# Performance work log

Measured on AMD Instinct MI355X. Metric: run time of the kernel, lower is better.

Reference implementation:

```python
import jax, jax.numpy as jnp
import numpy as np

EPS = 1e-5

def conv1x1(x, w, b):
    # x: [B,C,H,W], w: [O,C], b: [O]
    return jnp.einsum('bchw,oc->bohw', x, w) + b[None, :, None, None]

def bn(x, gamma, beta, mean, var):
    scale = gamma / jnp.sqrt(var + EPS)
    return x * scale[None, :, None, None] + (beta - mean * scale)[None, :, None, None]

def setup_inputs() -> dict:
    B, C, H, W = 8, 256, 64, 64
    F0, F1 = 128, 128
    key = jax.random.key(0)
    ks = jax.random.split(key, 16)
    d = {}
    d['inputs'] = jax.random.normal(ks[0], (B, C, H, W), dtype=jnp.float32)
    def make_cna(i, fout, fin):
        w = jax.random.normal(ks[i], (fout, fin), dtype=jnp.float32) / np.sqrt(fin)
        b = jnp.zeros((fout,), dtype=jnp.float32)
        g = jnp.ones((fout,), dtype=jnp.float32)
        be = jnp.zeros((fout,), dtype=jnp.float32)
        m = 0.1 * jax.random.normal(ks[i + 1], (fout,), dtype=jnp.float32)
        v = jax.random.uniform(ks[i + 2], (fout,), dtype=jnp.float32, minval=0.5, maxval=1.5)
        return w, b, g, be, m, v
    (d['theta_w'], d['theta_b'], d['theta_g'], d['theta_beta'], d['theta_m'], d['theta_v']) = make_cna(1, F0, C)
    (d['phi_w'], d['phi_b'], d['phi_g'], d['phi_beta'], d['phi_m'], d['phi_v']) = make_cna(4, F0, C)
    (d['mu_w'], d['mu_b'], d['mu_g'], d['mu_beta'], d['mu_m'], d['mu_v']) = make_cna(7, F1, C)
    d['pre_w'] = jax.random.normal(ks[10], (C, F1), dtype=jnp.float32) / np.sqrt(F1)
    d['pre_b'] = jnp.zeros((C,), dtype=jnp.float32)
    d['post_g'] = jnp.ones((C,), dtype=jnp.float32)
    d['post_beta'] = jnp.zeros((C,), dtype=jnp.float32)
    d['post_m'] = 0.1 * jax.random.normal(ks[11], (C,), dtype=jnp.float32)
    d['post_v'] = jax.random.uniform(ks[12], (C,), dtype=jnp.float32, minval=0.5, maxval=1.5)
    return d

def reference(inputs, theta_w, theta_b, theta_g, theta_beta, theta_m, theta_v,
              phi_w, phi_b, phi_g, phi_beta, phi_m, phi_v,
              mu_w, mu_b, mu_g, mu_beta, mu_m, mu_v,
              pre_w, pre_b, post_g, post_beta, post_m, post_v):
    B, C, H, W = inputs.shape
    N = H * W
    # theta/phi/mu: 1x1 conv + batchnorm (eval) + relu
    t = jax.nn.relu(bn(conv1x1(inputs, theta_w, theta_b), theta_g, theta_beta, theta_m, theta_v))
    p = jax.nn.relu(bn(conv1x1(inputs, phi_w, phi_b), phi_g, phi_beta, phi_m, phi_v))
    z = jax.nn.relu(bn(conv1x1(inputs, mu_w, mu_b), mu_g, mu_beta, mu_m, mu_v))
    tf = t.reshape(B, -1, N)   # [B,F0,N]
    pf = p.reshape(B, -1, N)   # [B,F0,N]
    zf = z.reshape(B, -1, N)   # [B,F1,N]
    # unscaled softmax(theta^T phi) mu^T, batched (original loops over B)
    attn = jax.nn.softmax(jnp.einsum('bfn,bfm->bnm', tf, pf), axis=-1)  # [B,N,N]
    u = jnp.einsum('bnm,bfm->bfn', attn, zf).reshape(B, -1, H, W)       # [B,F1,H,W]
    pre = conv1x1(u, pre_w, pre_b)                                       # [B,C,H,W]
    return jax.nn.relu(bn(pre + inputs, post_g, post_beta, post_m, post_v))
```

## Files before the change

kernel.cpp:

```cpp
#include <hip/hip_runtime.h>

typedef __attribute__((ext_vector_type(8))) _Float16 f16x8;
typedef __attribute__((ext_vector_type(4))) float f32x4;
typedef __attribute__((ext_vector_type(16))) float f32x16;
typedef __attribute__((ext_vector_type(4))) unsigned u32x4;
typedef __attribute__((ext_vector_type(2))) unsigned u32x2;

#define EPSV 1e-5f
#define BB 8
#define CC 256
#define NP 4096
#define FF 128
#define SPLIT 4
#define CHUNK 1024
#define NIT 32

#define GLD16(gp, lp) __builtin_amdgcn_global_load_lds( \
    (const __attribute__((address_space(1))) unsigned int*)(gp), \
    (__attribute__((address_space(3))) unsigned int*)(lp), 16, 0, 0)

static __device__ __forceinline__ unsigned short f2h(float f) {
    union { _Float16 h; unsigned short u; } v;
    v.h = (_Float16)f;
    return v.u;
}
static __device__ __forceinline__ float h2f(unsigned short u) {
    union { unsigned short u; _Float16 h; } v;
    v.u = u;
    return (float)v.h;
}
static __device__ __forceinline__ void plswap(unsigned& a, unsigned& b) {
    u32x2 r = __builtin_amdgcn_permlane32_swap(a, b, false, false);
    a = r[0]; b = r[1];
}
static __device__ __forceinline__ unsigned fbits(float f) { return __builtin_bit_cast(unsigned, f); }
static __device__ __forceinline__ float bitsf(unsigned u) { return __builtin_bit_cast(float, u); }

struct PrepArgs {
    const float* w[3]; const float* bias[3]; const float* g[3]; const float* be[3];
    const float* m[3]; const float* v[3];
    const float* pre_w; const float* pre_b;
    const float* post_g; const float* post_be; const float* post_m; const float* post_v;
    unsigned short* W_all; float* b_all; unsigned short* W2; float* b2; float* sres;
};

__global__ __launch_bounds__(256) void prep_kernel(PrepArgs a) {
    int idx = blockIdx.x * 256 + threadIdx.x;
    if (idx < 3 * 128 * 256) {
        int row = idx >> 8, c = idx & 255;
        int which = row >> 7, f = row & 127;
        float s = a.g[which][f] * rsqrtf(a.v[which][f] + EPSV);
        a.W_all[idx] = f2h(a.w[which][f * 256 + c] * s);
        if (c == 0)
            a.b_all[row] = s * a.bias[which][f] + a.be[which][f] - a.m[which][f] * s;
    } else {
        int i = idx - 3 * 128 * 256;
        if (i < 256 * 128) {
            int c = i >> 7, f = i & 127;
            float s = a.post_g[c] * rsqrtf(a.post_v[c] + EPSV);
            a.W2[i] = f2h(a.pre_w[i] * s);
            if (f == 0) {
                a.b2[c] = s * a.pre_b[c] + a.post_be[c] - a.post_m[c] * s;
                a.sres[c] = s;
            }
        }
    }
}

__global__ __launch_bounds__(256) void transpose_x_kernel(const float* __restrict__ x,
                                                          unsigned short* __restrict__ xT) {
    __shared__ float tile[64][65];
    int blk = blockIdx.x;
    int b  = blk >> 8;
    int c0 = ((blk >> 6) & 3) << 6;
    int n0 = (blk & 63) << 6;
    int t = threadIdx.x;
    const float* src = x + ((size_t)b * CC + c0) * NP + n0;
    #pragma unroll
    for (int i = 0; i < 16; ++i) {
        int cl = i * 4 + (t >> 6);
        tile[cl][t & 63] = src[(size_t)cl * NP + (t & 63)];
    }
    __syncthreads();
    unsigned short* dst = xT + ((size_t)b * NP + n0) * CC + c0;
    #pragma unroll
    for (int i = 0; i < 8; ++i) {
        int nl = i * 8 + (t >> 5);
        int cl = (t & 31) * 2;
        unsigned lo = f2h(tile[cl][nl]);
        unsigned hi = f2h(tile[cl + 1][nl]);
        *reinterpret_cast<unsigned*>(dst + (size_t)nl * CC + cl) = (hi << 16) | lo;
    }
}

__global__ __launch_bounds__(256) void qkv_kernel(const unsigned short* __restrict__ xT,
                                                  const unsigned short* __restrict__ W_all,
                                                  const float* __restrict__ b_all,
                                                  unsigned short* __restrict__ qT,
                                                  unsigned short* __restrict__ kT,
                                                  unsigned short* __restrict__ vT) {
    __shared__ unsigned short Alds[128 * 72];
    __shared__ unsigned short Blds[128 * 72];
    int blk = blockIdx.x;
    int b  = blk & 7;
    int r  = blk >> 3;
    int ft = r >> 5;
    int n0 = (r & 31) << 7;
    int fbase = ft << 7;
    int t = threadIdx.x, w = t >> 6, l = t & 63;
    int wr = (w >> 1) << 6, wc = (w & 1) << 6;
    const unsigned short* A  = xT + ((size_t)b * NP + n0) * CC;
    const unsigned short* Bw = W_all + (size_t)fbase * CC;

    f32x4 acc[4][4];
    #pragma unroll
    for (int i = 0; i < 4; ++i)
        #pragma unroll
        for (int j = 0; j < 4; ++j)
            acc[i][j] = f32x4{0.f, 0.f, 0.f, 0.f};

    for (int c0 = 0; c0 < 256; c0 += 64) {
        #pragma unroll
        for (int i = 0; i < 4; ++i) {
            int row = i * 32 + (t >> 3);
            int ch = (t & 7) * 8;
            *reinterpret_cast<int4*>(&Alds[row * 72 + ch]) =
                *reinterpret_cast<const int4*>(A + (size_t)row * CC + c0 + ch);
            *reinterpret_cast<int4*>(&Blds[row * 72 + ch]) =
                *reinterpret_cast<const int4*>(Bw + (size_t)row * CC + c0 + ch);
        }
        __syncthreads();
        #pragma unroll
        for (int kk = 0; kk < 2; ++kk) {
            f16x8 af[4], bfr[4];
            #pragma unroll
            for (int mi = 0; mi < 4; ++mi)
                af[mi] = *reinterpret_cast<const f16x8*>(
                    &Alds[(wr + mi * 16 + (l & 15)) * 72 + kk * 32 + (l >> 4) * 8]);
            #pragma unroll
            for (int ni = 0; ni < 4; ++ni)
                bfr[ni] = *reinterpret_cast<const f16x8*>(
                    &Blds[(wc + ni * 16 + (l & 15)) * 72 + kk * 32 + (l >> 4) * 8]);
            #pragma unroll
            for (int mi = 0; mi < 4; ++mi)
                #pragma unroll
                for (int ni = 0; ni < 4; ++ni)
                    acc[mi][ni] = __builtin_amdgcn_mfma_f32_16x16x32_f16(af[mi], bfr[ni], acc[mi][ni], 0, 0, 0);
        }
        __syncthreads();
    }

    #pragma unroll
    for (int mi = 0; mi < 4; ++mi) {
        #pragma unroll
        for (int ni = 0; ni < 4; ++ni) {
            int fl = wc + ni * 16 + (l & 15);
            float bias = b_all[fbase + fl];
            int nb = n0 + wr + mi * 16 + ((l >> 4) << 2);
            float v0 = acc[mi][ni][0] + bias; v0 = v0 > 0.f ? v0 : 0.f;
            float v1 = acc[mi][ni][1] + bias; v1 = v1 > 0.f ? v1 : 0.f;
            float v2 = acc[mi][ni][2] + bias; v2 = v2 > 0.f ? v2 : 0.f;
            float v3 = acc[mi][ni][3] + bias; v3 = v3 > 0.f ? v3 : 0.f;
            if (ft == 2) {
                int mtile = nb >> 5, kb = (nb >> 4) & 1, hh = (nb >> 3) & 1, j = nb & 7;
                int fb = fl >> 5, rcol = fl & 31;
                unsigned short* dst = vT + (size_t)b * NP * FF +
                    (size_t)mtile * 4096 + (size_t)(fb * 2 + kb) * 512 + (hh * 32 + rcol) * 8 + j;
                uint2 uu;
                uu.x = (unsigned)f2h(v0) | ((unsigned)f2h(v1) << 16);
                uu.y = (unsigned)f2h(v2) | ((unsigned)f2h(v3) << 16);
                *reinterpret_cast<uint2*>(dst) = uu;
            } else {
                unsigned short* dst = (ft == 0 ? qT : kT) + (size_t)b * NP * FF;
                int kf = fl >> 4, hh = (fl >> 3) & 1, j = fl & 7;
                unsigned short h0 = f2h(v0), h1 = f2h(v1), h2 = f2h(v2), h3 = f2h(v3);
                dst[(size_t)((nb + 0) >> 5) * 4096 + kf * 512 + (hh * 32 + ((nb + 0) & 31)) * 8 + j] = h0;
                dst[(size_t)((nb + 1) >> 5) * 4096 + kf * 512 + (hh * 32 + ((nb + 1) & 31)) * 8 + j] = h1;
                dst[(size_t)((nb + 2) >> 5) * 4096 + kf * 512 + (hh * 32 + ((nb + 2) & 31)) * 8 + j] = h2;
                dst[(size_t)((nb + 3) >> 5) * 4096 + kf * 512 + (hh * 32 + ((nb + 3) & 31)) * 8 + j] = h3;
            }
        }
    }
}

__global__ __launch_bounds__(256, 3) void attn_kernel(const unsigned short* __restrict__ qT,
                                                      const unsigned short* __restrict__ kT,
                                                      const unsigned short* __restrict__ vT,
                                                      unsigned short* __restrict__ Uh,
                                                      float2* __restrict__ ml) {
    __shared__ unsigned short Vl[2][4096];
    int blk = blockIdx.x;
    int b = blk & 7;
    int rest = blk >> 3;
    int s = rest & 3;
    int qt = rest >> 2;
    int t = threadIdx.x, w = t >> 6, l = t & 63;
    int r = l & 31, h = l >> 5;
    int n0w = qt * 128 + w * 32;
    const unsigned short* Qb = qT + (size_t)b * NP * FF + (size_t)(qt * 4 + w) * 4096;
    const unsigned short* Kb = kT + (size_t)b * NP * FF + (size_t)(s * 32) * 4096;
    const unsigned short* Vb = vT + (size_t)b * NP * FF + (size_t)(s * 32) * 4096;

    f16x8 qf[8], kg[8];
    #pragma unroll
    for (int kf = 0; kf < 8; ++kf) {
        qf[kf] = *reinterpret_cast<const f16x8*>(Qb + kf * 512 + l * 8);
        kg[kf] = *reinterpret_cast<const f16x8*>(Kb + kf * 512 + l * 8);
    }
    GLD16(Vb + w * 512 + l * 8, &Vl[0][w * 512]);
    GLD16(Vb + 2048 + w * 512 + l * 8, &Vl[0][2048 + w * 512]);

    f32x16 U[4];
    #pragma unroll
    for (int fb = 0; fb < 4; ++fb)
        #pragma unroll
        for (int i = 0; i < 16; ++i) U[fb][i] = 0.f;
    float mrun = -1e30f, lrun = 0.f;

    int cur = 0;
    for (int it = 0; it < NIT; ++it) {
        asm volatile("s_waitcnt vmcnt(0)" ::: "memory");
        __builtin_amdgcn_s_barrier();
        asm volatile("" ::: "memory");
        if (it + 1 < NIT) {
            const unsigned short* vn = Vb + (size_t)(it + 1) * 4096;
            GLD16(vn + w * 512 + l * 8, &Vl[cur ^ 1][w * 512]);
            GLD16(vn + 2048 + w * 512 + l * 8, &Vl[cur ^ 1][2048 + w * 512]);
        }

        f32x16 St;
        #pragma unroll
        for (int i = 0; i < 16; ++i) St[i] = 0.f;
        __builtin_amdgcn_s_setprio(1);
        #pragma unroll
        for (int kf = 0; kf < 8; ++kf)
            St = __builtin_amdgcn_mfma_f32_32x32x16_f16(kg[kf], qf[kf], St, 0, 0, 0);
        __builtin_amdgcn_s_setprio(0);

        if (it + 1 < NIT) {
            const unsigned short* kn = Kb + (size_t)(it + 1) * 4096;
            #pragma unroll
            for (int kf = 0; kf < 8; ++kf)
                kg[kf] = *reinterpret_cast<const f16x8*>(kn + kf * 512 + l * 8);
        }

        float pm0 = fmaxf(fmaxf(St[0], St[1]), fmaxf(St[2], St[3]));
        float pm1 = fmaxf(fmaxf(St[4], St[5]), fmaxf(St[6], St[7]));
        float pm2 = fmaxf(fmaxf(St[8], St[9]), fmaxf(St[10], St[11]));
        float pm3 = fmaxf(fmaxf(St[12], St[13]), fmaxf(St[14], St[15]));
        float pmax = fmaxf(fmaxf(pm0, pm1), fmaxf(pm2, pm3));
        { unsigned pa = fbits(pmax), pb = pa; plswap(pa, pb); pmax = fmaxf(bitsf(pa), bitsf(pb)); }
        if (__any(pmax > mrun + 8.0f)) {
            float mnew = fmaxf(mrun, pmax);
            float sc = __expf(mrun - mnew);
            mrun = mnew; lrun *= sc;
            #pragma unroll
            for (int rr = 0; rr < 16; ++rr) {
                float scb = __shfl(sc, (rr & 3) + 8 * (rr >> 2) + 4 * h);
                U[0][rr] *= scb; U[1][rr] *= scb; U[2][rr] *= scb; U[3][rr] *= scb;
            }
        }
        float lsum = 0.f;
        unsigned pk[8];
        #pragma unroll
        for (int i = 0; i < 8; ++i) {
            float e0 = __expf(St[2 * i] - mrun);
            float e1 = __expf(St[2 * i + 1] - mrun);
            lsum += e0 + e1;
            pk[i] = __builtin_bit_cast(unsigned, __builtin_amdgcn_cvt_pkrtz(e0, e1));
        }
        { unsigned la = fbits(lsum), lb = la; plswap(la, lb); lsum = bitsf(la) + bitsf(lb); }
        lrun += lsum;

        const unsigned short* Vc = &Vl[cur][0];
        __builtin_amdgcn_s_setprio(1);
        #pragma unroll
        for (int kb = 0; kb < 2; ++kb) {
            unsigned a0 = pk[kb * 4 + 0], b0 = pk[kb * 4 + 2];
            unsigned a1 = pk[kb * 4 + 1], b1 = pk[kb * 4 + 3];
            plswap(a0, b0);
            plswap(a1, b1);
            u32x4 du; du[0] = a0; du[1] = a1; du[2] = b0; du[3] = b1;
            f16x8 af = __builtin_bit_cast(f16x8, du);
            #pragma unroll
            for (int fb = 0; fb < 4; ++fb) {
                f16x8 vf = *reinterpret_cast<const f16x8*>(Vc + (fb * 2 + kb) * 512 + l * 8);
                U[fb] = __builtin_amdgcn_mfma_f32_32x32x16_f16(af, vf, U[fb], 0, 0, 0);
            }
        }
        __builtin_amdgcn_s_setprio(0);
        cur ^= 1;
    }

    float linv = 1.0f / lrun;
    unsigned short* up = Uh + (size_t)(s * 8 + b) * NP * FF;
    #pragma unroll
    for (int rr = 0; rr < 16; ++rr) {
        int nn = (rr & 3) + 8 * (rr >> 2) + 4 * h;
        float scb = __shfl(linv, nn);
        int n = n0w + nn;
        #pragma unroll
        for (int fb = 0; fb < 4; ++fb)
            up[(size_t)n * FF + fb * 32 + r] = f2h(U[fb][rr] * scb);
    }
    if (l < 32)
        ml[(size_t)(s * 8 + b) * NP + n0w + l] = make_float2(mrun, lrun);
}

__global__ __launch_bounds__(256) void combine_kernel(const unsigned short* __restrict__ Uh,
                                                      const float2* __restrict__ ml,
                                                      unsigned short* __restrict__ uT) {
    int row = blockIdx.x * 2 + (threadIdx.x >> 7);
    int f = threadIdx.x & 127;
    float m[SPLIT], lv[SPLIT];
    #pragma unroll
    for (int s = 0; s < SPLIT; ++s) {
        float2 v = ml[(size_t)s * (BB * NP) + row];
        m[s] = v.x; lv[s] = v.y;
    }
    float M = fmaxf(fmaxf(m[0], m[1]), fmaxf(m[2], m[3]));
    float wsum = 0.f, acc = 0.f;
    #pragma unroll
    for (int s = 0; s < SPLIT; ++s) {
        float wgt = __expf(m[s] - M) * lv[s];
        wsum += wgt;
        acc += wgt * h2f(Uh[((size_t)s * (BB * NP) + row) * FF + f]);
    }
    uT[(size_t)row * FF + f] = f2h(acc / wsum);
}

__global__ __launch_bounds__(256) void final_kernel(const unsigned short* __restrict__ uT,
                                                    const unsigned short* __restrict__ W2,
                                                    const float* __restrict__ b2,
                                                    const float* __restrict__ sres,
                                                    const float* __restrict__ x,
                                                    float* __restrict__ out) {
    __shared__ unsigned short Alds[128 * 72];
    __shared__ unsigned short Blds[128 * 72];
    int blk = blockIdx.x;
    int b  = blk & 7;
    int r  = blk >> 3;
    int ct = r & 1;
    int nt = r >> 1;
    int c0 = ct << 7, n0 = nt << 7;
    int t = threadIdx.x, w = t >> 6, l = t & 63;
    int wr = (w >> 1) << 6, wc = (w & 1) << 6;

    f32x4 acc[4][4];
    #pragma unroll
    for (int i = 0; i < 4; ++i)
        #pragma unroll
        for (int j = 0; j < 4; ++j)
            acc[i][j] = f32x4{0.f, 0.f, 0.f, 0.f};

    for (int k0 = 0; k0 < 128; k0 += 64) {
        #pragma unroll
        for (int i = 0; i < 4; ++i) {
            int row = i * 32 + (t >> 3);
            int ch = (t & 7) * 8;
            *reinterpret_cast<int4*>(&Alds[row * 72 + ch]) =
                *reinterpret_cast<const int4*>(W2 + (size_t)(c0 + row) * FF + k0 + ch);
            *reinterpret_cast<int4*>(&Blds[row * 72 + ch]) =
                *reinterpret_cast<const int4*>(uT + ((size_t)b * NP + n0 + row) * FF + k0 + ch);
        }
        __syncthreads();
        #pragma unroll
        for (int kk = 0; kk < 2; ++kk) {
            f16x8 af[4], bfr[4];
            #pragma unroll
            for (int mi = 0; mi < 4; ++mi)
                af[mi] = *reinterpret_cast<const f16x8*>(
                    &Alds[(wr + mi * 16 + (l & 15)) * 72 + kk * 32 + (l >> 4) * 8]);
            #pragma unroll
            for (int ni = 0; ni < 4; ++ni)
                bfr[ni] = *reinterpret_cast<const f16x8*>(
                    &Blds[(wc + ni * 16 + (l & 15)) * 72 + kk * 32 + (l >> 4) * 8]);
            #pragma unroll
            for (int mi = 0; mi < 4; ++mi)
                #pragma unroll
                for (int ni = 0; ni < 4; ++ni)
                    acc[mi][ni] = __builtin_amdgcn_mfma_f32_16x16x32_f16(af[mi], bfr[ni], acc[mi][ni], 0, 0, 0);
        }
        __syncthreads();
    }

    const float* xb = x + (size_t)b * CC * NP;
    float* ob = out + (size_t)b * CC * NP;
    #pragma unroll
    for (int mi = 0; mi < 4; ++mi)
        #pragma unroll
        for (int ni = 0; ni < 4; ++ni) {
            int n = n0 + wc + ni * 16 + (l & 15);
            int cb = c0 + wr + mi * 16 + ((l >> 4) << 2);
            #pragma unroll
            for (int rg = 0; rg < 4; ++rg) {
                int c = cb + rg;
                float v = acc[mi][ni][rg] + b2[c] + sres[c] * xb[(size_t)c * NP + n];
                ob[(size_t)c * NP + n] = v > 0.f ? v : 0.f;
            }
        }
}

extern "C" void kernel_launch(void* const* d_in, const int* in_sizes, int n_in,
                              void* d_out, int out_size, void* d_ws, size_t ws_size,
                              hipStream_t stream) {
    const float* x = (const float*)d_in[0];
    char* ws = (char*)d_ws;
    unsigned short* W_all = (unsigned short*)(ws);
    float*          b_all = (float*)(ws + 196608);
    unsigned short* W2    = (unsigned short*)(ws + 198144);
    float*          b2    = (float*)(ws + 263680);
    float*          sres  = (float*)(ws + 264704);
    unsigned short* xT    = (unsigned short*)(ws + 265728);
    unsigned short* qT    = (unsigned short*)(ws + 17042944);
    unsigned short* kT    = (unsigned short*)(ws + 25431552);
    unsigned short* vT    = (unsigned short*)(ws + 33820160);
    unsigned short* uT    = (unsigned short*)(ws + 42208768);
    unsigned short* Uh    = (unsigned short*)(ws + 50597376);
    float2*         ml    = (float2*)(ws + 84151808);

    PrepArgs pa;
    pa.w[0]  = (const float*)d_in[1];  pa.bias[0] = (const float*)d_in[2];
    pa.g[0]  = (const float*)d_in[3];  pa.be[0]   = (const float*)d_in[4];
    pa.m[0]  = (const float*)d_in[5];  pa.v[0]    = (const float*)d_in[6];
    pa.w[1]  = (const float*)d_in[7];  pa.bias[1] = (const float*)d_in[8];
    pa.g[1]  = (const float*)d_in[9];  pa.be[1]   = (const float*)d_in[10];
    pa.m[1]  = (const float*)d_in[11]; pa.v[1]    = (const float*)d_in[12];
    pa.w[2]  = (const float*)d_in[13]; pa.bias[2] = (const float*)d_in[14];
    pa.g[2]  = (const float*)d_in[15]; pa.be[2]   = (const float*)d_in[16];
    pa.m[2]  = (const float*)d_in[17]; pa.v[2]    = (const float*)d_in[18];
    pa.pre_w = (const float*)d_in[19]; pa.pre_b   = (const float*)d_in[20];
    pa.post_g = (const float*)d_in[21]; pa.post_be = (const float*)d_in[22];
    pa.post_m = (const float*)d_in[23]; pa.post_v  = (const float*)d_in[24];
    pa.W_all = W_all; pa.b_all = b_all; pa.W2 = W2; pa.b2 = b2; pa.sres = sres;

    prep_kernel<<<dim3(512), dim3(256), 0, stream>>>(pa);
    transpose_x_kernel<<<dim3(2048), dim3(256), 0, stream>>>(x, xT);
    qkv_kernel<<<dim3(768), dim3(256), 0, stream>>>(xT, W_all, b_all, qT, kT, vT);
    attn_kernel<<<dim3(1024), dim3(256), 0, stream>>>(qT, kT, vT, Uh, ml);
    combine_kernel<<<dim3(16384), dim3(256), 0, stream>>>(Uh, ml, uT);
    final_kernel<<<dim3(512), dim3(256), 0, stream>>>(uT, W2, b2, sres, x, (float*)d_out);
}
```

Measured before the change: 271.7 us.

## Fold log2e into theta weights, use raw exp2, split MFMA chains, relax vmcnt wait

```diff
diff --git a/kernel.cpp b/kernel.cpp
--- a/kernel.cpp
+++ b/kernel.cpp
@@ -14,6 +14,7 @@
 #define SPLIT 4
 #define CHUNK 1024
 #define NIT 32
+#define LOG2E 1.4426950408889634f
 
 #define GLD16(gp, lp) __builtin_amdgcn_global_load_lds( \
     (const __attribute__((address_space(1))) unsigned int*)(gp), \
@@ -35,6 +36,11 @@
 }
 static __device__ __forceinline__ unsigned fbits(float f) { return __builtin_bit_cast(unsigned, f); }
 static __device__ __forceinline__ float bitsf(unsigned u) { return __builtin_bit_cast(float, u); }
+static __device__ __forceinline__ float fexp2(float x) {
+    float r;
+    asm("v_exp_f32 %0, %1" : "=v"(r) : "v"(x));
+    return r;
+}
 
 struct PrepArgs {
     const float* w[3]; const float* bias[3]; const float* g[3]; const float* be[3];
@@ -50,9 +56,11 @@
         int row = idx >> 8, c = idx & 255;
         int which = row >> 7, f = row & 127;
         float s = a.g[which][f] * rsqrtf(a.v[which][f] + EPSV);
+        float bb = s * a.bias[which][f] + a.be[which][f] - a.m[which][f] * s;
+        if (which == 0) { s *= LOG2E; bb *= LOG2E; }
         a.W_all[idx] = f2h(a.w[which][f * 256 + c] * s);
         if (c == 0)
-            a.b_all[row] = s * a.bias[which][f] + a.be[which][f] - a.m[which][f] * s;
+            a.b_all[row] = bb;
     } else {
         int i = idx - 3 * 128 * 256;
         if (i < 256 * 128) {
@@ -201,14 +209,16 @@
     const unsigned short* Kb = kT + (size_t)b * NP * FF + (size_t)(s * 32) * 4096;
     const unsigned short* Vb = vT + (size_t)b * NP * FF + (size_t)(s * 32) * 4096;
 
+    GLD16(Vb + w * 512 + l * 8, &Vl[0][w * 512]);
+    GLD16(Vb + 2048 + w * 512 + l * 8, &Vl[0][2048 + w * 512]);
+    __builtin_amdgcn_sched_barrier(0);
+
     f16x8 qf[8], kg[8];
     #pragma unroll
     for (int kf = 0; kf < 8; ++kf) {
         qf[kf] = *reinterpret_cast<const f16x8*>(Qb + kf * 512 + l * 8);
         kg[kf] = *reinterpret_cast<const f16x8*>(Kb + kf * 512 + l * 8);
     }
-    GLD16(Vb + w * 512 + l * 8, &Vl[0][w * 512]);
-    GLD16(Vb + 2048 + w * 512 + l * 8, &Vl[0][2048 + w * 512]);
 
     f32x16 U[4];
     #pragma unroll
@@ -219,7 +229,8 @@
 
     int cur = 0;
     for (int it = 0; it < NIT; ++it) {
-        asm volatile("s_waitcnt vmcnt(0)" ::: "memory");
+        asm volatile("s_waitcnt vmcnt(8)" ::: "memory");
+        __builtin_amdgcn_sched_barrier(0);
         __builtin_amdgcn_s_barrier();
         asm volatile("" ::: "memory");
         if (it + 1 < NIT) {
@@ -227,14 +238,17 @@
             GLD16(vn + w * 512 + l * 8, &Vl[cur ^ 1][w * 512]);
             GLD16(vn + 2048 + w * 512 + l * 8, &Vl[cur ^ 1][2048 + w * 512]);
         }
-
-        f32x16 St;
-        #pragma unroll
-        for (int i = 0; i < 16; ++i) St[i] = 0.f;
+        __builtin_amdgcn_sched_barrier(0);
+
+        f32x16 StA, StB;
+        #pragma unroll
+        for (int i = 0; i < 16; ++i) { StA[i] = 0.f; StB[i] = 0.f; }
         __builtin_amdgcn_s_setprio(1);
         #pragma unroll
-        for (int kf = 0; kf < 8; ++kf)
-            St = __builtin_amdgcn_mfma_f32_32x32x16_f16(kg[kf], qf[kf], St, 0, 0, 0);
+        for (int kf = 0; kf < 4; ++kf) {
+            StA = __builtin_amdgcn_mfma_f32_32x32x16_f16(kg[2 * kf],     qf[2 * kf],     StA, 0, 0, 0);
+            StB = __builtin_amdgcn_mfma_f32_32x32x16_f16(kg[2 * kf + 1], qf[2 * kf + 1], StB, 0, 0, 0);
+        }
         __builtin_amdgcn_s_setprio(0);
 
         if (it + 1 < NIT) {
@@ -244,15 +258,21 @@
                 kg[kf] = *reinterpret_cast<const f16x8*>(kn + kf * 512 + l * 8);
         }
 
-        float pm0 = fmaxf(fmaxf(St[0], St[1]), fmaxf(St[2], St[3]));
-        float pm1 = fmaxf(fmaxf(St[4], St[5]), fmaxf(St[6], St[7]));
-        float pm2 = fmaxf(fmaxf(St[8], St[9]), fmaxf(St[10], St[11]));
-        float pm3 = fmaxf(fmaxf(St[12], St[13]), fmaxf(St[14], St[15]));
-        float pmax = fmaxf(fmaxf(pm0, pm1), fmaxf(pm2, pm3));
+        #pragma unroll
+        for (int i = 0; i < 16; ++i) StA[i] += StB[i];
+
+        float a0 = fmaxf(fmaxf(StA[0], StA[1]), StA[2]);
+        float a1 = fmaxf(fmaxf(StA[3], StA[4]), StA[5]);
+        float a2 = fmaxf(fmaxf(StA[6], StA[7]), StA[8]);
+        float a3 = fmaxf(fmaxf(StA[9], StA[10]), StA[11]);
+        float a4 = fmaxf(fmaxf(StA[12], StA[13]), StA[14]);
+        float b0 = fmaxf(fmaxf(a0, a1), a2);
+        float b1 = fmaxf(fmaxf(a3, a4), StA[15]);
+        float pmax = fmaxf(b0, b1);
         { unsigned pa = fbits(pmax), pb = pa; plswap(pa, pb); pmax = fmaxf(bitsf(pa), bitsf(pb)); }
-        if (__any(pmax > mrun + 8.0f)) {
+        if (__any(pmax > mrun + 11.0f)) {
             float mnew = fmaxf(mrun, pmax);
-            float sc = __expf(mrun - mnew);
+            float sc = fexp2(mrun - mnew);
             mrun = mnew; lrun *= sc;
             #pragma unroll
             for (int rr = 0; rr < 16; ++rr) {
@@ -264,8 +284,8 @@
         unsigned pk[8];
         #pragma unroll
         for (int i = 0; i < 8; ++i) {
-            float e0 = __expf(St[2 * i] - mrun);
-            float e1 = __expf(St[2 * i + 1] - mrun);
+            float e0 = fexp2(StA[2 * i] - mrun);
+            float e1 = fexp2(StA[2 * i + 1] - mrun);
             lsum += e0 + e1;
             pk[i] = __builtin_bit_cast(unsigned, __builtin_amdgcn_cvt_pkrtz(e0, e1));
         }
@@ -276,11 +296,11 @@
         __builtin_amdgcn_s_setprio(1);
         #pragma unroll
         for (int kb = 0; kb < 2; ++kb) {
-            unsigned a0 = pk[kb * 4 + 0], b0 = pk[kb * 4 + 2];
-            unsigned a1 = pk[kb * 4 + 1], b1 = pk[kb * 4 + 3];
-            plswap(a0, b0);
-            plswap(a1, b1);
-            u32x4 du; du[0] = a0; du[1] = a1; du[2] = b0; du[3] = b1;
+            unsigned c0 = pk[kb * 4 + 0], d0 = pk[kb * 4 + 2];
+            unsigned c1 = pk[kb * 4 + 1], d1 = pk[kb * 4 + 3];
+            plswap(c0, d0);
+            plswap(c1, d1);
+            u32x4 du; du[0] = c0; du[1] = c1; du[2] = d0; du[3] = d1;
             f16x8 af = __builtin_bit_cast(f16x8, du);
             #pragma unroll
             for (int fb = 0; fb < 4; ++fb) {
@@ -322,7 +342,7 @@
     float wsum = 0.f, acc = 0.f;
     #pragma unroll
     for (int s = 0; s < SPLIT; ++s) {
-        float wgt = __expf(m[s] - M) * lv[s];
+        float wgt = fexp2(m[s] - M) * lv[s];
         wsum += wgt;
         acc += wgt * h2f(Uh[((size_t)s * (BB * NP) + row) * FF + f]);
     }
```

Result: slower. 278.8 us (+2.6%).
